# Kernel optimization log

Hardware: AMD Instinct MI355X
Metric: run time of the kernel (lower is better)

The kernel has to match this reference:

```python
import jax, jax.numpy as jnp
import numpy as np

N, S, T, E, H = 4, 2048, 2048, 512, 8
HD = E // H  # head_dim = 64


def setup_inputs() -> dict:
    key0 = jax.random.key(0)
    ks = jax.random.split(key0, 12)
    sc = 1.0 / np.sqrt(E)
    inp = {
        "query": jax.random.normal(ks[0], (N, S, E), jnp.float32),
        "key": jax.random.normal(ks[1], (N, T, E), jnp.float32),
        "value": jax.random.normal(ks[2], (N, T, E), jnp.float32),
        "attn_mask": jnp.tril(jnp.ones((S, T), jnp.int32)),  # causal: 0 => masked
        # nn.Linear weights (out, in) and biases, torch convention y = x @ W.T + b
        "Wq": jax.random.normal(ks[3], (E, E), jnp.float32) * sc,
        "bq": jax.random.normal(ks[4], (E,), jnp.float32) * sc,
        "Wk": jax.random.normal(ks[5], (E, E), jnp.float32) * sc,
        "bk": jax.random.normal(ks[6], (E,), jnp.float32) * sc,
        "Wv": jax.random.normal(ks[7], (E, E), jnp.float32) * sc,
        "bv": jax.random.normal(ks[8], (E,), jnp.float32) * sc,
        "Wp": jax.random.normal(ks[9], (E, E), jnp.float32) * sc,
        "bp": jax.random.normal(ks[10], (E,), jnp.float32) * sc,
    }
    return inp


def reference(query, key, value, attn_mask, Wq, bq, Wk, bk, Wv, bv, Wp, bp):
    # QKV projections, split heads: (N, H, L, HD)
    q = (query @ Wq.T + bq).reshape(N, S, H, HD).transpose(0, 2, 1, 3)
    k = (key @ Wk.T + bk).reshape(N, T, H, HD).transpose(0, 2, 1, 3)
    v = (value @ Wv.T + bv).reshape(N, T, H, HD).transpose(0, 2, 1, 3)
    # scaled scores (N, H, S, T) -- intentionally materialized like the original
    e = jnp.einsum("nhsd,nhtd->nhst", q, k) / jnp.sqrt(jnp.float32(HD))
    e = jnp.where(attn_mask == 0, -jnp.inf, e)
    a = jax.nn.softmax(e, axis=-1)
    # dropout is identity in eval mode (reference runs deterministic/eval)
    y = jnp.einsum("nhst,nhtd->nhsd", a, v)
    y = y.transpose(0, 2, 1, 3).reshape(N, S, E)
    return y @ Wp.T + bp
```

## Files before the change

kernel.cpp:

```cpp
#include <hip/hip_runtime.h>


#define DEV __device__ __forceinline__

typedef unsigned short u16;
typedef unsigned int u32;
typedef __bf16 bf16x8 __attribute__((ext_vector_type(8)));
typedef float f32x4 __attribute__((ext_vector_type(4)));

#define MFMA_BF16(A, B, C) __builtin_amdgcn_mfma_f32_16x16x32_bf16(A, B, C, 0, 0, 0)

DEV u16 f2bf(float f) {
  u32 u = __builtin_bit_cast(u32, f);
  u += 0x7fffu + ((u >> 16) & 1u);
  return (u16)(u >> 16);
}

DEV void cp16(void* l, const void* g) {
  __builtin_amdgcn_global_load_lds(
      (const __attribute__((address_space(1))) u32*)g,
      (__attribute__((address_space(3))) u32*)l, 16, 0, 0);
}

#define WAIT_VM(N) asm volatile("s_waitcnt vmcnt(" #N ")" ::: "memory")
#define WAIT_VMLG  asm volatile("s_waitcnt vmcnt(0) lgkmcnt(0)" ::: "memory")
#define WAIT_LG    asm volatile("s_waitcnt lgkmcnt(0)" ::: "memory")
#define BARRIER    asm volatile("s_barrier" ::: "memory")

__global__ __launch_bounds__(256) void cast_all(
    const float* __restrict__ q, const float* __restrict__ k, const float* __restrict__ v,
    const float* __restrict__ wq, const float* __restrict__ wk,
    const float* __restrict__ wv, const float* __restrict__ wp,
    u16* qo, u16* ko, u16* vo, u16* wqo, u16* wko, u16* wvo, u16* wpo) {
  int b = blockIdx.x;
  const float* s;
  u16* d;
  int i;
  if (b < 12288) {
    int t = b >> 12;
    s = (t == 0) ? q : (t == 1) ? k : v;
    d = (t == 0) ? qo : (t == 1) ? ko : vo;
    i = (b & 4095) * 256 + threadIdx.x;
  } else {
    int t = (b - 12288) >> 8;
    s = (t == 0) ? wq : (t == 1) ? wk : (t == 2) ? wv : wp;
    d = (t == 0) ? wqo : (t == 1) ? wko : (t == 2) ? wvo : wpo;
    i = ((b - 12288) & 255) * 256 + threadIdx.x;
  }
  float4 f = ((const float4*)s)[i];
  ushort4 o;
  o.x = f2bf(f.x); o.y = f2bf(f.y); o.z = f2bf(f.z); o.w = f2bf(f.w);
  ((ushort4*)d)[i] = o;
}

DEV void gemm_stage(const u16* __restrict__ A, const u16* __restrict__ W,
                    u16* As, u16* Bs, int m0, int n0, int kt, int tid) {
#pragma unroll
  for (int i = 0; i < 2; ++i) {
    int c = tid + 256 * i;
    int row = c >> 2, kc = (c & 3) * 8;
    cp16(&As[c * 8], A + (m0 + row) * 512 + kt + kc);
    cp16(&Bs[c * 8], W + (n0 + row) * 512 + kt + kc);
  }
}

DEV void gemm_loop(const u16* __restrict__ A, const u16* __restrict__ W,
                   u16* As, u16* Bs,
                   int m0, int n0, int tid, f32x4 acc[4][4]) {
  const int lane = tid & 63, wid = tid >> 6;
  const int wm = wid & 1, wn = wid >> 1;
  const int l15 = lane & 15, l4 = lane >> 4;
  gemm_stage(A, W, As, Bs, m0, n0, 0, tid);
  gemm_stage(A, W, As + 4096, Bs + 4096, m0, n0, 32, tid);
  WAIT_VM(4);
  BARRIER;
  for (int it = 0; it < 16; ++it) {
    const u16* Ac = As + (it & 1) * 4096;
    const u16* Bc = Bs + (it & 1) * 4096;
    bf16x8 af[4], bfr[4];
#pragma unroll
    for (int f = 0; f < 4; ++f) {
      af[f]  = *(const bf16x8*)&Ac[(wm * 64 + f * 16 + l15) * 32 + l4 * 8];
      bfr[f] = *(const bf16x8*)&Bc[(wn * 64 + f * 16 + l15) * 32 + l4 * 8];
    }
    __builtin_amdgcn_s_setprio(1);
#pragma unroll
    for (int fm = 0; fm < 4; ++fm)
#pragma unroll
      for (int fn = 0; fn < 4; ++fn)
        acc[fm][fn] = MFMA_BF16(af[fm], bfr[fn], acc[fm][fn]);
    __builtin_amdgcn_s_setprio(0);
    if (it < 15) {
      WAIT_VMLG;
      BARRIER;
      if (it + 2 < 16)
        gemm_stage(A, W, As + (it & 1) * 4096, Bs + (it & 1) * 4096,
                   m0, n0, (it + 2) * 32, tid);
    }
  }
}

__global__ __launch_bounds__(256) void gemm_qkv(
    const u16* __restrict__ qx, const u16* __restrict__ kx, const u16* __restrict__ vx,
    const u16* __restrict__ wq, const u16* __restrict__ wk, const u16* __restrict__ wv,
    const float* __restrict__ bq, const float* __restrict__ bk, const float* __restrict__ bv,
    u16* qp, u16* kp, u16* vtO) {
  __shared__ u16 As[2 * 128 * 32];
  __shared__ u16 Bs[2 * 128 * 32];
  const int wsel = blockIdx.x >> 2;
  const u16* A = (wsel == 0) ? qx : (wsel == 1) ? kx : vx;
  const u16* W = (wsel == 0) ? wq : (wsel == 1) ? wk : wv;
  const float* bias = (wsel == 0) ? bq : (wsel == 1) ? bk : bv;
  const int n0 = (blockIdx.x & 3) * 128, m0 = blockIdx.y * 128;
  const int tid = threadIdx.x, lane = tid & 63, wid = tid >> 6;
  const int wm = wid & 1, wn = wid >> 1;
  const int l15 = lane & 15, l4 = lane >> 4;

  f32x4 acc[4][4] = {};
  gemm_loop(A, W, As, Bs, m0, n0, tid, acc);

  if (wsel == 2) {
#pragma unroll
    for (int fn = 0; fn < 4; ++fn) {
      int col = n0 + wn * 64 + fn * 16 + l15;
      float bvv = bias[col];
      int h = col >> 6, d = col & 63;
#pragma unroll
      for (int fm = 0; fm < 4; ++fm) {
        int rowb = m0 + wm * 64 + fm * 16 + l4 * 4;
        int nb = rowb >> 11, t = rowb & 2047;
        int t64 = t & 63, tt = t >> 6;
        int tg = ((t64 >> 5) << 2) | ((t64 >> 2) & 3);
        int j0 = ((t64 >> 4) & 1) << 2;
        ushort4 o;
        o.x = f2bf(acc[fm][fn][0] + bvv);
        o.y = f2bf(acc[fm][fn][1] + bvv);
        o.z = f2bf(acc[fm][fn][2] + bvv);
        o.w = f2bf(acc[fm][fn][3] + bvv);
        *(ushort4*)&vtO[((nb * 8 + h) * 64 + d) * 2048 + tt * 64 + tg * 8 + j0] = o;
      }
    }
  } else {
    u16* C = (wsel == 0) ? qp : kp;
    const float osc = (wsel == 0) ? 0.18033688f : 1.0f;
#pragma unroll
    for (int fn = 0; fn < 4; ++fn) {
      int col = n0 + wn * 64 + fn * 16 + l15;
      float bvv = bias[col];
#pragma unroll
      for (int fm = 0; fm < 4; ++fm) {
        int rowb = m0 + wm * 64 + fm * 16 + l4 * 4;
#pragma unroll
        for (int r = 0; r < 4; ++r)
          C[(rowb + r) * 512 + col] = f2bf((acc[fm][fn][r] + bvv) * osc);
      }
    }
  }
}

__global__ __launch_bounds__(256) void gemm_out(const u16* __restrict__ A,
                                                const u16* __restrict__ W,
                                                const float* __restrict__ bias,
                                                float* __restrict__ C) {
  __shared__ u16 As[2 * 64 * 32];
  __shared__ u16 Bs[2 * 128 * 32];
  const int n0 = blockIdx.x * 128, m0 = blockIdx.y * 64;
  const int tid = threadIdx.x, lane = tid & 63, wid = tid >> 6;
  const int wm = wid & 1, wn = wid >> 1;
  const int l15 = lane & 15, l4 = lane >> 4;

  auto stage = [&](u16* Asb, u16* Bsb, int kt) {
    {
      int row = tid >> 2, kc = (tid & 3) * 8;
      cp16(&Asb[tid * 8], A + (m0 + row) * 512 + kt + kc);
    }
#pragma unroll
    for (int i = 0; i < 2; ++i) {
      int c = tid + 256 * i;
      int row = c >> 2, kc = (c & 3) * 8;
      cp16(&Bsb[c * 8], W + (n0 + row) * 512 + kt + kc);
    }
  };

  f32x4 acc[2][4] = {};
  stage(As, Bs, 0);
  stage(As + 2048, Bs + 4096, 32);
  WAIT_VM(3);
  BARRIER;
  for (int it = 0; it < 16; ++it) {
    const u16* Ac = As + (it & 1) * 2048;
    const u16* Bc = Bs + (it & 1) * 4096;
    bf16x8 af[2], bfr[4];
#pragma unroll
    for (int f = 0; f < 2; ++f)
      af[f] = *(const bf16x8*)&Ac[(wm * 32 + f * 16 + l15) * 32 + l4 * 8];
#pragma unroll
    for (int f = 0; f < 4; ++f)
      bfr[f] = *(const bf16x8*)&Bc[(wn * 64 + f * 16 + l15) * 32 + l4 * 8];
    __builtin_amdgcn_s_setprio(1);
#pragma unroll
    for (int fm = 0; fm < 2; ++fm)
#pragma unroll
      for (int fn = 0; fn < 4; ++fn)
        acc[fm][fn] = MFMA_BF16(af[fm], bfr[fn], acc[fm][fn]);
    __builtin_amdgcn_s_setprio(0);
    if (it < 15) {
      WAIT_VMLG;
      BARRIER;
      if (it + 2 < 16)
        stage(As + (it & 1) * 2048, Bs + (it & 1) * 4096, (it + 2) * 32);
    }
  }

#pragma unroll
  for (int fn = 0; fn < 4; ++fn) {
    int col = n0 + wn * 64 + fn * 16 + l15;
    float bvv = bias[col];
#pragma unroll
    for (int fm = 0; fm < 2; ++fm) {
      int rowb = m0 + wm * 32 + fm * 16 + l4 * 4;
#pragma unroll
      for (int r = 0; r < 4; ++r)
        C[(rowb + r) * 512 + col] = acc[fm][fn][r] + bvv;
    }
  }
}

__global__ __launch_bounds__(256) void attn_kernel(const u16* __restrict__ Qg,
                                                   const u16* __restrict__ Kg,
                                                   const u16* __restrict__ Vt,
                                                   u16* __restrict__ Yg,
                                                   float* __restrict__ Opart,
                                                   float* __restrict__ Lpart) {
  __shared__ u16 Qs[64 * 64];
  __shared__ u16 Ks[128 * 64];
  __shared__ u16 Vts[64 * 128];

  const int bid = blockIdx.x;
  int qt, nh, it0 = 0, half = 0;
  bool split;
  if (bid < 512) {
    qt = 16 + (bid >> 5); nh = bid & 31; split = true;
  } else if (bid < 576) {
    int i = bid - 512; qt = 14 + (i >> 5); nh = i & 31; split = false;
  } else if (bid < 640) {
    int i = bid - 576; qt = 30 + (i >> 5); nh = i & 31; it0 = 8; half = 1; split = true;
  } else {
    int g = bid - 640, c = 7 - (g >> 7), k = g & 127;
    if (k < 64) { qt = 2 * c - 2 + (k >> 5); nh = k & 31; split = false; }
    else { int k2 = k - 64; qt = 2 * c + 14 + (k2 >> 5); nh = k2 & 31; it0 = 8; half = 1; split = true; }
  }
  const int nt = (qt >> 1) + 1;
  const int itEnd = (split && half == 0) ? 8 : nt;

  const int n = nh >> 3, h = nh & 7;
  const int tid = threadIdx.x, lane = tid & 63, w = tid >> 6;
  const int l15 = lane & 15, l4 = lane >> 4;
  const int s0 = qt * 64;

  const u16* Qb = Qg + (n * 2048 + s0) * 512 + h * 64;
  const u16* Kb = Kg + n * 2048 * 512 + h * 64;
  const u16* Vb = Vt + nh * 64 * 2048;

  const u16* kSrc[4];
  const u16* vSrc[4];
  int kDst[4], vDst[4];
#pragma unroll
  for (int i = 0; i < 4; ++i) {
    int c = tid + 256 * i;
    int t = c >> 3, dg = (c & 7) ^ (t & 7);
    kSrc[i] = Kb + (it0 * 128 + t) * 512 + dg * 8;
    kDst[i] = c * 8;
    int d = c >> 4, x = c & 15;
    vSrc[i] = Vb + d * 2048 + it0 * 128 + ((x ^ (d & 15)) * 8);
    vDst[i] = c * 8;
  }

#pragma unroll
  for (int i = 0; i < 2; ++i) {
    int c = tid + 256 * i;
    int row = c >> 3, dg = (c & 7) ^ (row & 7);
    cp16(&Qs[c * 8], Qb + row * 512 + dg * 8);
  }
#pragma unroll
  for (int i = 0; i < 4; ++i) { cp16(&Ks[kDst[i]], kSrc[i]); kSrc[i] += 128 * 512; }
#pragma unroll
  for (int i = 0; i < 4; ++i) { cp16(&Vts[vDst[i]], vSrc[i]); vSrc[i] += 128; }

  WAIT_VM(8);
  BARRIER;
  const int qr = w * 16 + l15;
  bf16x8 qf0 = *(const bf16x8*)&Qs[qr * 64 + ((l4 ^ (qr & 7)) * 8)];
  bf16x8 qf1 = *(const bf16x8*)&Qs[qr * 64 + (((4 + l4) ^ (qr & 7)) * 8)];
  WAIT_VM(4);
  BARRIER;

  f32x4 accO[4] = {};
  f32x4 lacc = {};
  const int sgl = s0 + w * 16 + l15;

  for (int it = it0; it < itEnd; ++it) {
    const int t0 = it * 128;
    const bool more = (it + 1 < itEnd);

    f32x4 st[8];
    __builtin_amdgcn_s_setprio(1);
#pragma unroll
    for (int fn = 0; fn < 8; ++fn) {
      int tr = fn * 16 + l15;
      bf16x8 k0 = *(const bf16x8*)&Ks[tr * 64 + ((l4 ^ (tr & 7)) * 8)];
      bf16x8 k1 = *(const bf16x8*)&Ks[tr * 64 + (((4 + l4) ^ (tr & 7)) * 8)];
      f32x4 a = {};
      a = MFMA_BF16(k0, qf0, a);
      st[fn] = MFMA_BF16(k1, qf1, a);
    }
    __builtin_amdgcn_s_setprio(0);

    WAIT_VMLG;
    BARRIER;
    if (more) {
#pragma unroll
      for (int i = 0; i < 4; ++i) { cp16(&Ks[kDst[i]], kSrc[i]); kSrc[i] += 128 * 512; }
    }

    const bool diag = (t0 + 128 > s0);
    if (diag) {
#pragma unroll
      for (int fn = 0; fn < 8; ++fn)
#pragma unroll
        for (int r = 0; r < 4; ++r) {
          int tg = t0 + fn * 16 + l4 * 4 + r;
          if (tg > sgl) st[fn][r] = -1e30f;
        }
    }
#pragma unroll
    for (int fn = 0; fn < 8; ++fn)
#pragma unroll
      for (int r = 0; r < 4; ++r)
        st[fn][r] = __builtin_amdgcn_exp2f(st[fn][r]);
    {
      f32x4 s4 = st[0] + st[1];
      s4 += st[2] + st[3];
      s4 += st[4] + st[5];
      s4 += st[6] + st[7];
      lacc += s4;
    }

    bf16x8 pa[4];
#pragma unroll
    for (int ks = 0; ks < 4; ++ks) {
      bf16x8 t;
      t[0] = (__bf16)st[2 * ks][0];     t[1] = (__bf16)st[2 * ks][1];
      t[2] = (__bf16)st[2 * ks][2];     t[3] = (__bf16)st[2 * ks][3];
      t[4] = (__bf16)st[2 * ks + 1][0]; t[5] = (__bf16)st[2 * ks + 1][1];
      t[6] = (__bf16)st[2 * ks + 1][2]; t[7] = (__bf16)st[2 * ks + 1][3];
      pa[ks] = t;
    }

    __builtin_amdgcn_s_setprio(1);
#pragma unroll
    for (int ks = 0; ks < 4; ++ks) {
#pragma unroll
      for (int fd = 0; fd < 4; ++fd) {
        int d = fd * 16 + l15;
        bf16x8 bv = *(const bf16x8*)&Vts[d * 128 + (((ks * 4 + l4) ^ l15) * 8)];
        accO[fd] = MFMA_BF16(pa[ks], bv, accO[fd]);
      }
    }
    __builtin_amdgcn_s_setprio(0);

    if (more) {
      WAIT_VMLG;
      BARRIER;
#pragma unroll
      for (int i = 0; i < 4; ++i) { cp16(&Vts[vDst[i]], vSrc[i]); vSrc[i] += 128; }
    }
  }

  float lr = lacc[0] + lacc[1] + lacc[2] + lacc[3];
  lr += __shfl_xor(lr, 16);
  lr += __shfl_xor(lr, 32);

  if (!split) {
    float lO[4];
#pragma unroll
    for (int r = 0; r < 4; ++r) lO[r] = __shfl(lr, (lane & 48) | (l4 * 4 + r));
#pragma unroll
    for (int fd = 0; fd < 4; ++fd)
#pragma unroll
      for (int r = 0; r < 4; ++r) {
        int row = s0 + w * 16 + l4 * 4 + r;
        int col = h * 64 + fd * 16 + l15;
        Yg[(n * 2048 + row) * 512 + col] = f2bf(accO[fd][r] / lO[r]);
      }
  } else {
    const int p = (qt - 16) * 32 + nh;
    float* Ob = Opart + (p * 2 + half) * 4096;
#pragma unroll
    for (int fd = 0; fd < 4; ++fd)
#pragma unroll
      for (int r = 0; r < 4; ++r)
        Ob[(fd * 4 + r) * 256 + tid] = accO[fd][r];
    if (l4 == 0) Lpart[(p * 2 + half) * 64 + w * 16 + l15] = lr;
  }
}

__global__ __launch_bounds__(256) void merge_o(const float* __restrict__ Opart,
                                               const float* __restrict__ Lpart,
                                               u16* __restrict__ Yg) {
  const int p = blockIdx.x;
  const int qt = 16 + (p >> 5), nh = p & 31;
  const int n = nh >> 3, h = nh & 7, s0 = qt * 64;
  const int tid = threadIdx.x, lane = tid & 63, w = tid >> 6;
  const int l15 = lane & 15, l4 = lane >> 4;
  const float* O1 = Opart + p * 8192;
  const float* O2 = O1 + 4096;
  const float* L1 = Lpart + p * 128;
  const float* L2 = L1 + 64;
  float lO[4];
#pragma unroll
  for (int r = 0; r < 4; ++r) {
    int row = w * 16 + l4 * 4 + r;
    lO[r] = L1[row] + L2[row];
  }
#pragma unroll
  for (int fd = 0; fd < 4; ++fd)
#pragma unroll
    for (int r = 0; r < 4; ++r) {
      float o = O1[(fd * 4 + r) * 256 + tid] + O2[(fd * 4 + r) * 256 + tid];
      int row = s0 + w * 16 + l4 * 4 + r;
      int col = h * 64 + fd * 16 + l15;
      Yg[(n * 2048 + row) * 512 + col] = f2bf(o / lO[r]);
    }
}

extern "C" void kernel_launch(void* const* d_in, const int* in_sizes, int n_in,
                              void* d_out, int out_size, void* d_ws, size_t ws_size,
                              hipStream_t stream) {
  (void)in_sizes; (void)n_in; (void)out_size; (void)ws_size;
  const float* query = (const float*)d_in[0];
  const float* key_  = (const float*)d_in[1];
  const float* value = (const float*)d_in[2];
  const float* Wq = (const float*)d_in[4];
  const float* bq = (const float*)d_in[5];
  const float* Wk = (const float*)d_in[6];
  const float* bk = (const float*)d_in[7];
  const float* Wv = (const float*)d_in[8];
  const float* bv = (const float*)d_in[9];
  const float* Wp = (const float*)d_in[10];
  const float* bp = (const float*)d_in[11];

  char* ws = (char*)d_ws;
  u16* qx  = (u16*)(ws);
  u16* kx  = (u16*)(ws + 8388608);
  u16* vx  = (u16*)(ws + 16777216);
  u16* wqx = (u16*)(ws + 25165824);
  u16* wkx = (u16*)(ws + 25690112);
  u16* wvx = (u16*)(ws + 26214400);
  u16* wpx = (u16*)(ws + 26738688);
  u16* qp  = (u16*)(ws + 27262976);
  u16* kp  = (u16*)(ws + 35651584);
  u16* vt  = (u16*)(ws + 44040192);
  u16* y   = qx;
  float* Opart = (float*)kx;
  float* Lpart = (float*)wqx;

  cast_all<<<13312, 256, 0, stream>>>(query, key_, value, Wq, Wk, Wv, Wp,
                                      qx, kx, vx, wqx, wkx, wvx, wpx);
  gemm_qkv<<<dim3(12, 64), 256, 0, stream>>>(qx, kx, vx, wqx, wkx, wvx,
                                             bq, bk, bv, qp, kp, vt);
  attn_kernel<<<1536, 256, 0, stream>>>(qp, kp, vt, y, Opart, Lpart);
  merge_o<<<512, 256, 0, stream>>>(Opart, Lpart, y);
  gemm_out<<<dim3(4, 128), 256, 0, stream>>>(y, wpx, bp, (float*)d_out);
}
```

Baseline: 190.7 us.

## Stage V-transpose epilogue through LDS and load Q fragments directly from global

The V projection epilogue now writes bias-added bf16 results into a padded shared-memory tile and then stores them to the transposed V buffer with coalesced 16-byte rows, replacing scattered 8-byte stores. The attention kernel drops its Q shared-memory staging and loads each lane's Q fragments straight from global memory into registers, which removes one barrier and some LDS. The GEMM's shared buffer grows to hold the padded tile. The direct Q loads are less coalesced, and the V path adds two barriers.

New measurement: 191.2 us. About the same (+0.2%).

```diff
diff --git a/kernel.cpp b/kernel.cpp
--- a/kernel.cpp
+++ b/kernel.cpp
@@ -105,8 +105,9 @@
     const u16* __restrict__ wq, const u16* __restrict__ wk, const u16* __restrict__ wv,
     const float* __restrict__ bq, const float* __restrict__ bk, const float* __restrict__ bv,
     u16* qp, u16* kp, u16* vtO) {
-  __shared__ u16 As[2 * 128 * 32];
-  __shared__ u16 Bs[2 * 128 * 32];
+  __shared__ u16 SH[17408];
+  u16* As = SH;
+  u16* Bs = SH + 8192;
   const int wsel = blockIdx.x >> 2;
   const u16* A = (wsel == 0) ? qx : (wsel == 1) ? kx : vx;
   const u16* W = (wsel == 0) ? wq : (wsel == 1) ? wk : wv;
@@ -120,25 +121,36 @@
   gemm_loop(A, W, As, Bs, m0, n0, tid, acc);
 
   if (wsel == 2) {
+    WAIT_LG;
+    BARRIER;
+    u16* Cs = SH;
 #pragma unroll
     for (int fn = 0; fn < 4; ++fn) {
-      int col = n0 + wn * 64 + fn * 16 + l15;
-      float bvv = bias[col];
-      int h = col >> 6, d = col & 63;
+      int dl = wn * 64 + fn * 16 + l15;
+      float bvv = bias[n0 + dl];
 #pragma unroll
       for (int fm = 0; fm < 4; ++fm) {
-        int rowb = m0 + wm * 64 + fm * 16 + l4 * 4;
-        int nb = rowb >> 11, t = rowb & 2047;
-        int t64 = t & 63, tt = t >> 6;
-        int tg = ((t64 >> 5) << 2) | ((t64 >> 2) & 3);
-        int j0 = ((t64 >> 4) & 1) << 2;
+        int trow = wm * 64 + fm * 16 + l4 * 4;
+        int t64 = trow & 63;
+        int pbase = (trow >> 6) * 64 + ((((t64 >> 5) << 2) | ((t64 >> 2) & 3)) << 3)
+                    + (((t64 >> 4) & 1) << 2);
         ushort4 o;
         o.x = f2bf(acc[fm][fn][0] + bvv);
         o.y = f2bf(acc[fm][fn][1] + bvv);
         o.z = f2bf(acc[fm][fn][2] + bvv);
         o.w = f2bf(acc[fm][fn][3] + bvv);
-        *(ushort4*)&vtO[((nb * 8 + h) * 64 + d) * 2048 + tt * 64 + tg * 8 + j0] = o;
+        *(ushort4*)&Cs[dl * 136 + pbase] = o;
       }
+    }
+    WAIT_LG;
+    BARRIER;
+    const int nb = m0 >> 11, m0loc = m0 & 2047;
+#pragma unroll
+    for (int i = 0; i < 8; ++i) {
+      int f = i * 256 + tid;
+      int rowd = f >> 4, ch = (f & 15) * 8;
+      uint4 x = *(const uint4*)&Cs[rowd * 136 + ch];
+      *(uint4*)(vtO + (nb * 512 + n0 + rowd) * 2048 + m0loc + ch) = x;
     }
   } else {
     u16* C = (wsel == 0) ? qp : kp;
@@ -232,7 +244,6 @@
                                                    u16* __restrict__ Yg,
                                                    float* __restrict__ Opart,
                                                    float* __restrict__ Lpart) {
-  __shared__ u16 Qs[64 * 64];
   __shared__ u16 Ks[128 * 64];
   __shared__ u16 Vts[64 * 128];
 
@@ -258,9 +269,13 @@
   const int l15 = lane & 15, l4 = lane >> 4;
   const int s0 = qt * 64;
 
-  const u16* Qb = Qg + (n * 2048 + s0) * 512 + h * 64;
   const u16* Kb = Kg + n * 2048 * 512 + h * 64;
   const u16* Vb = Vt + nh * 64 * 2048;
+
+  const int qr = w * 16 + l15;
+  const u16* qptr = Qg + (n * 2048 + s0 + qr) * 512 + h * 64;
+  bf16x8 qf0 = __builtin_bit_cast(bf16x8, *(const uint4*)(qptr + l4 * 8));
+  bf16x8 qf1 = __builtin_bit_cast(bf16x8, *(const uint4*)(qptr + 32 + l4 * 8));
 
   const u16* kSrc[4];
   const u16* vSrc[4];
@@ -277,21 +292,10 @@
   }
 
 #pragma unroll
-  for (int i = 0; i < 2; ++i) {
-    int c = tid + 256 * i;
-    int row = c >> 3, dg = (c & 7) ^ (row & 7);
-    cp16(&Qs[c * 8], Qb + row * 512 + dg * 8);
-  }
-#pragma unroll
   for (int i = 0; i < 4; ++i) { cp16(&Ks[kDst[i]], kSrc[i]); kSrc[i] += 128 * 512; }
 #pragma unroll
   for (int i = 0; i < 4; ++i) { cp16(&Vts[vDst[i]], vSrc[i]); vSrc[i] += 128; }
 
-  WAIT_VM(8);
-  BARRIER;
-  const int qr = w * 16 + l15;
-  bf16x8 qf0 = *(const bf16x8*)&Qs[qr * 64 + ((l4 ^ (qr & 7)) * 8)];
-  bf16x8 qf1 = *(const bf16x8*)&Qs[qr * 64 + (((4 + l4) ^ (qr & 7)) * 8)];
   WAIT_VM(4);
   BARRIER;
 
```
